# Kernel optimization log

Measured on AMD Instinct MI355X. Metric: run time of the kernel, lower is better.

The kernel has to match this reference:

```python
import jax, jax.numpy as jnp
import numpy as np

B, T, CH, V, E, L = 64, 1024, 256, 32000, 64, 128  # batch, enc_len, channel, vocab, emb_dim, latent_dims


def setup_inputs() -> dict:
    key = jax.random.key(0)
    ks = jax.random.split(key, 13)
    s = 0.05  # weight init scale
    return {
        "prev_cont_vec": jax.random.normal(ks[0], (B, CH), jnp.float32),
        "F": jax.random.normal(ks[1], (B, T, CH), jnp.float32),
        "prev_char": jax.random.normal(ks[2], (B, V), jnp.float32),
        "state_h": jax.random.normal(ks[3], (B, L), jnp.float32),
        "state_c": jax.random.normal(ks[4], (B, L), jnp.float32),
        # learned parameters (all Dense layers use_bias=False)
        "Wc": jax.random.normal(ks[5], (V, E), jnp.float32) * s,
        "Wct1": jax.random.normal(ks[6], (CH, E), jnp.float32) * s,
        "Wo": jax.random.normal(ks[7], (L, V), jnp.float32) * s,
        "Wct2": jax.random.normal(ks[8], (CH, V), jnp.float32) * s,
        "lstm_kernel": jax.random.normal(ks[9], (E, 4 * L), jnp.float32) * s,
        "lstm_recurrent": jax.random.normal(ks[10], (L, 4 * L), jnp.float32) * s,
        "W_h": jax.random.normal(ks[11], (L, CH), jnp.float32) * s,
        "V_attn": jax.random.normal(ks[12], (1, 1, CH), jnp.float32) * s,
    }


def reference(prev_cont_vec, F, prev_char, state_h, state_c,
              Wc, Wct1, Wo, Wct2, lstm_kernel, lstm_recurrent, W_h, V_attn):
    # lstm input: Wc(prev_char) + Wct1(prev_cont_vec)  -> [B, E]
    lstm_inp = prev_char @ Wc + prev_cont_vec @ Wct1
    # Keras LSTMCell (no bias), gate order i, f, c, o
    z = lstm_inp @ lstm_kernel + state_h @ lstm_recurrent  # [B, 4L]
    zi, zf, zg, zo = jnp.split(z, 4, axis=-1)
    i = jax.nn.sigmoid(zi)
    f = jax.nn.sigmoid(zf)
    g = jnp.tanh(zg)
    o = jax.nn.sigmoid(zo)
    new_c = f * state_c + i * g
    new_h = o * jnp.tanh(new_c)
    # training=True branch: clip returned cell state
    new_c_out = jnp.clip(new_c, -10.0, 10.0)
    # additive attention over time axis of F [B, T, CH]
    H_tfm = (new_h @ W_h)[:, None, :]            # [B, 1, CH]
    e_t = V_attn * jnp.tanh(H_tfm + F)           # [B, T, CH]
    attn = jax.nn.softmax(e_t, axis=1)           # softmax over T, per channel
    c_t = jnp.sum(attn * F, axis=1)              # [B, CH]
    # output distribution
    O_t = jax.nn.softmax(new_h @ Wo + c_t @ Wct2, axis=1)  # [B, V]
    return (O_t, c_t, new_h, new_c_out)
```

## Files before the change

kernel.cpp:

```cpp
#include <hip/hip_runtime.h>
#include <hip/hip_bf16.h>

#define BB 64
#define TT 1024
#define CHN 256
#define VV 32000
#define EE 64
#define LL 128
#define NC1 250
#define KC1 128
#define TS 32
#define NV5 500

typedef unsigned short u16;
typedef unsigned int u32;
typedef __attribute__((ext_vector_type(8))) short short8;
typedef __attribute__((ext_vector_type(16))) float f32x16;

__device__ __forceinline__ float fast_rcp(float x) { return __builtin_amdgcn_rcpf(x); }
__device__ __forceinline__ float tanh_fast(float y) {
    float e = __expf(2.0f * y);
    return 1.0f - 2.0f * fast_rcp(1.0f + e);
}
__device__ __forceinline__ float sigmoid_fast(float x) {
    return fast_rcp(1.0f + __expf(-x));
}
__device__ __forceinline__ u16 f2bf(float f) {
    u32 u = __float_as_uint(f);
    return (u16)((u + 0x7fffu + ((u >> 16) & 1u)) >> 16);
}
__device__ __forceinline__ u32 pack_bf2(float lo, float hi) {
    return (u32)f2bf(lo) | ((u32)f2bf(hi) << 16);
}
__device__ __forceinline__ float bf2f(u16 x) {
    return __uint_as_float(((u32)x) << 16);
}
__device__ __forceinline__ size_t apk_idx(int g, int b) {
    return ((size_t)(((g >> 3) * 2 + ((g & 7) >> 2)) * 64 + b)) * 4 + (g & 3);
}

__global__ __launch_bounds__(512) void k1_stage1(const float* __restrict__ A,
                                                 const float* __restrict__ Wc,
                                                 float* __restrict__ part) {
    __shared__ float sW[KC1][EE];
    __shared__ float sAT[KC1][64];
    const int kc = blockIdx.x;
    const int k0 = kc * KC1;
    const int t  = threadIdx.x;

    #pragma unroll
    for (int f = t; f < 2048; f += 512)
        *(float4*)(&sW[0][0] + f * 4) = *(const float4*)(Wc + (size_t)k0 * EE + f * 4);
    {
        const int bl = t & 63;
        const int kq = t >> 6;
        const float* src = A + (size_t)bl * VV + k0 + kq * 16;
        #pragma unroll
        for (int j4 = 0; j4 < 4; ++j4) {
            float4 v = *(const float4*)(src + j4 * 4);
            sAT[kq * 16 + j4 * 4 + 0][bl] = v.x;
            sAT[kq * 16 + j4 * 4 + 1][bl] = v.y;
            sAT[kq * 16 + j4 * 4 + 2][bl] = v.z;
            sAT[kq * 16 + j4 * 4 + 3][bl] = v.w;
        }
    }
    __syncthreads();

    const int e  = t & 63;
    const int b0 = (t >> 6) * 8;
    float acc[8];
    #pragma unroll
    for (int i = 0; i < 8; ++i) acc[i] = 0.0f;

    #pragma unroll 4
    for (int k = 0; k < KC1; ++k) {
        float wt = sW[k][e];
        float4 a0 = *(const float4*)&sAT[k][b0];
        float4 a1 = *(const float4*)&sAT[k][b0 + 4];
        acc[0] = fmaf(a0.x, wt, acc[0]);
        acc[1] = fmaf(a0.y, wt, acc[1]);
        acc[2] = fmaf(a0.z, wt, acc[2]);
        acc[3] = fmaf(a0.w, wt, acc[3]);
        acc[4] = fmaf(a1.x, wt, acc[4]);
        acc[5] = fmaf(a1.y, wt, acc[5]);
        acc[6] = fmaf(a1.z, wt, acc[6]);
        acc[7] = fmaf(a1.w, wt, acc[7]);
    }
    #pragma unroll
    for (int i = 0; i < 8; ++i)
        part[((size_t)(b0 + i) * NC1 + kc) * EE + e] = acc[i];
}

__global__ __launch_bounds__(512) void k2_lstm(const float* __restrict__ part,
    const float* __restrict__ pcv, const float* __restrict__ state_h,
    const float* __restrict__ state_c, const float* __restrict__ Wct1,
    const float* __restrict__ lstm_kernel, const float* __restrict__ lstm_rec,
    const float* __restrict__ W_h,
    float* __restrict__ out_newh, float* __restrict__ out_newc,
    u32* __restrict__ Apk, float* __restrict__ Htfm) {
    __shared__ float red[8][EE];
    __shared__ float inp[EE];
    __shared__ float sh[LL];
    __shared__ float z[4 * LL];
    __shared__ float nh[LL];
    const int b = blockIdx.x;
    const int t = threadIdx.x;
    const int e  = t & 63;
    const int g  = t >> 6;

    {
        float s = 0.0f;
        #pragma unroll 4
        for (int j = g; j < NC1; j += 8)
            s += part[((size_t)b * NC1 + j) * EE + e];
        const int c0 = g * 32;
        #pragma unroll 8
        for (int c = 0; c < 32; ++c)
            s = fmaf(pcv[b * CHN + c0 + c], Wct1[(size_t)(c0 + c) * EE + e], s);
        red[g][e] = s;
    }
    __syncthreads();
    if (t < EE) {
        float s = 0.0f;
        #pragma unroll
        for (int j = 0; j < 8; ++j) s += red[j][t];
        inp[t] = s;
    } else if (t >= 64 && t < 64 + LL) {
        sh[t - 64] = state_h[b * LL + (t - 64)];
    }
    __syncthreads();
    {
        float a = 0.0f;
        #pragma unroll 8
        for (int e2 = 0; e2 < EE; ++e2) a = fmaf(inp[e2], lstm_kernel[e2 * 512 + t], a);
        #pragma unroll 8
        for (int l = 0; l < LL; ++l) a = fmaf(sh[l], lstm_rec[l * 512 + t], a);
        z[t] = a;
    }
    __syncthreads();
    if (t < LL) {
        float zi = z[t], zf = z[LL + t], zg = z[2 * LL + t], zo = z[3 * LL + t];
        float ig = sigmoid_fast(zi);
        float fg = sigmoid_fast(zf);
        float gg = tanh_fast(zg);
        float og = sigmoid_fast(zo);
        float co = state_c[b * LL + t];
        float cn = fg * co + ig * gg;
        float hn = og * tanh_fast(cn);
        out_newc[b * LL + t] = fminf(fmaxf(cn, -10.0f), 10.0f);
        out_newh[b * LL + t] = hn;
        nh[t] = hn;
    }
    __syncthreads();
    if (t < CHN) {
        float a = 0.0f;
        #pragma unroll 8
        for (int l = 0; l < LL; ++l) a = fmaf(nh[l], W_h[l * CHN + t], a);
        Htfm[b * CHN + t] = a;
    } else if (t >= CHN && t < CHN + 64) {
        const int gp = t - CHN;
        Apk[apk_idx(gp, b)] = pack_bf2(nh[2 * gp], nh[2 * gp + 1]);
    }
}

__global__ __launch_bounds__(256) void k3_attn(const float* __restrict__ F,
    const float* __restrict__ Htfm, const float* __restrict__ Vattn,
    float* __restrict__ pS, float* __restrict__ pW) {
    __shared__ float4 sS[256];
    __shared__ float4 sW[256];
    const int b    = blockIdx.x;
    const int ts   = blockIdx.y;
    const int lane = threadIdx.x & 63;
    const int w    = threadIdx.x >> 6;
    const int ch   = lane * 4;

    float4 h = *(const float4*)(Htfm + b * CHN + ch);
    float4 v = *(const float4*)(Vattn + ch);
    float s0 = 0, s1 = 0, s2 = 0, s3 = 0;
    float a0 = 0, a1 = 0, a2 = 0, a3 = 0;

    const float* Fp = F + ((size_t)b * TT + ts * (TT / TS) + w * 8) * CHN + ch;
    float4 cur = *(const float4*)(Fp);
    #pragma unroll
    for (int t = 0; t < 8; ++t) {
        float4 nxt;
        if (t < 7) nxt = *(const float4*)(Fp + (size_t)(t + 1) * CHN);
        float e0 = __expf(v.x * tanh_fast(h.x + cur.x));
        float e1 = __expf(v.y * tanh_fast(h.y + cur.y));
        float e2 = __expf(v.z * tanh_fast(h.z + cur.z));
        float e3 = __expf(v.w * tanh_fast(h.w + cur.w));
        s0 += e0; s1 += e1; s2 += e2; s3 += e3;
        a0 = fmaf(e0, cur.x, a0); a1 = fmaf(e1, cur.y, a1);
        a2 = fmaf(e2, cur.z, a2); a3 = fmaf(e3, cur.w, a3);
        cur = nxt;
    }
    sS[threadIdx.x] = make_float4(s0, s1, s2, s3);
    sW[threadIdx.x] = make_float4(a0, a1, a2, a3);
    __syncthreads();
    if (threadIdx.x < 64) {
        float4 S = sS[threadIdx.x];
        float4 W = sW[threadIdx.x];
        #pragma unroll
        for (int j = 1; j < 4; ++j) {
            float4 s = sS[j * 64 + threadIdx.x];
            float4 q = sW[j * 64 + threadIdx.x];
            S.x += s.x; S.y += s.y; S.z += s.z; S.w += s.w;
            W.x += q.x; W.y += q.y; W.z += q.z; W.w += q.w;
        }
        int base = (b * TS + ts) * CHN + threadIdx.x * 4;
        *(float4*)(pS + base) = S;
        *(float4*)(pW + base) = W;
    }
}

__global__ __launch_bounds__(256) void k4_combine(const float* __restrict__ pS,
    const float* __restrict__ pW, float* __restrict__ out_ct, u32* __restrict__ Apk) {
    __shared__ float sc[CHN];
    const int b = blockIdx.x;
    const int ch = threadIdx.x;
    float S = 0.0f, W = 0.0f;
    #pragma unroll
    for (int j = 0; j < TS; ++j) {
        int idx = (b * TS + j) * CHN + ch;
        S += pS[idx];
        W += pW[idx];
    }
    float c = W / S;
    out_ct[b * CHN + ch] = c;
    sc[ch] = c;
    __syncthreads();
    if (ch < 128)
        Apk[apk_idx(64 + ch, b)] = pack_bf2(sc[2 * ch], sc[2 * ch + 1]);
}

__global__ __launch_bounds__(256) void k5_logits(const float* __restrict__ Wo,
    const float* __restrict__ Wct2, const u32* __restrict__ Apk,
    u16* __restrict__ expb, float* __restrict__ psum) {
    __shared__ float rp[4][32];
    const int t    = threadIdx.x;
    const int lane = t & 63;
    const int wv   = t >> 6;
    const int m    = lane & 31;
    const int kq   = lane >> 5;
    const int vt   = blockIdx.x;
    const int n0   = vt * 64 + (wv >> 1) * 32;
    const int gb0  = (wv & 1) * 32;

    uint4 af[24];
    #pragma unroll
    for (int tt = 0; tt < 24; ++tt)
        af[tt] = *(const uint4*)&Apk[((size_t)((tt * 2 + kq) * 64) + gb0 + m) * 4];

    f32x16 acc = {0.0f, 0.0f, 0.0f, 0.0f, 0.0f, 0.0f, 0.0f, 0.0f,
                  0.0f, 0.0f, 0.0f, 0.0f, 0.0f, 0.0f, 0.0f, 0.0f};

    float wbuf[3][8];
    #pragma unroll
    for (int pf = 0; pf < 2; ++pf) {
        const float* c0 = Wo + (size_t)(pf * 16 + kq * 8) * VV + n0 + m;
        #pragma unroll
        for (int j = 0; j < 8; ++j) wbuf[pf][j] = c0[(size_t)j * VV];
    }

    #pragma unroll
    for (int tt = 0; tt < 24; ++tt) {
        if (tt < 22) {
            const int kn = (tt + 2) * 16 + kq * 8;
            const float* cn = (kn < LL ? Wo + (size_t)kn * VV
                                       : Wct2 + (size_t)(kn - LL) * VV) + n0 + m;
            #pragma unroll
            for (int j = 0; j < 8; ++j) wbuf[(tt + 2) % 3][j] = cn[(size_t)j * VV];
        }
        short8 a, b;
        u32 ax = af[tt].x, ay = af[tt].y, az = af[tt].z, aw = af[tt].w;
        #pragma unroll
        for (int r = 0; r < 4; ++r) {
            u32 lo = __float_as_uint(wbuf[tt % 3][2 * r]);
            u32 hi = __float_as_uint(wbuf[tt % 3][2 * r + 1]);
            u32 bp = (lo >> 16) | (hi & 0xffff0000u);
            u32 ap = (r == 0) ? ax : (r == 1) ? ay : (r == 2) ? az : aw;
            a[2 * r]     = (short)(ap & 0xffff);
            a[2 * r + 1] = (short)(ap >> 16);
            b[2 * r]     = (short)(bp & 0xffff);
            b[2 * r + 1] = (short)(bp >> 16);
        }
        acc = __builtin_amdgcn_mfma_f32_32x32x16_bf16(a, b, acc, 0, 0, 0);
    }

    float ex[16];
    #pragma unroll
    for (int r = 0; r < 16; ++r) {
        const int row = (r & 3) + 8 * (r >> 2) + 4 * kq;
        ex[r] = __expf(acc[r]);
        expb[(size_t)(gb0 + row) * VV + n0 + m] = f2bf(ex[r]);
    }
    #pragma unroll
    for (int r = 0; r < 16; ++r) {
        float s = ex[r];
        s += __shfl_xor(s, 1, 64);  s += __shfl_xor(s, 2, 64);
        s += __shfl_xor(s, 4, 64);  s += __shfl_xor(s, 8, 64);
        s += __shfl_xor(s, 16, 64);
        ex[r] = s;
    }
    if (m == 0) {
        #pragma unroll
        for (int r = 0; r < 16; ++r)
            rp[wv][(r & 3) + 8 * (r >> 2) + 4 * kq] = ex[r];
    }
    __syncthreads();
    if (t < 64) {
        const int hb = t >> 5, r = t & 31;
        psum[(size_t)vt * BB + t] = rp[hb][r] + rp[2 + hb][r];
    }
}

__global__ __launch_bounds__(256) void k5c_norm(const u16* __restrict__ expb,
    const float* __restrict__ psum, float* __restrict__ O) {
    __shared__ float red[256];
    const int b   = blockIdx.x;
    const int seg = blockIdx.y;
    const int t   = threadIdx.x;

    float s = psum[(size_t)t * BB + b];
    if (t + 256 < NV5) s += psum[(size_t)(t + 256) * BB + b];
    red[t] = s;
    __syncthreads();
    #pragma unroll
    for (int off = 128; off > 0; off >>= 1) {
        if (t < off) red[t] += red[t + off];
        __syncthreads();
    }
    const float inv = fast_rcp(red[0]);

    const u16* src = expb + (size_t)b * VV + seg * 4000;
    float* dst     = O + (size_t)b * VV + seg * 4000;
    #pragma unroll 2
    for (int i = t; i < 1000; i += 256) {
        uint2 pk = *(const uint2*)(src + i * 4);
        float4 f;
        f.x = bf2f((u16)(pk.x & 0xffff)) * inv;
        f.y = bf2f((u16)(pk.x >> 16)) * inv;
        f.z = bf2f((u16)(pk.y & 0xffff)) * inv;
        f.w = bf2f((u16)(pk.y >> 16)) * inv;
        *(float4*)(dst + i * 4) = f;
    }
}

extern "C" void kernel_launch(void* const* d_in, const int* in_sizes, int n_in,
                              void* d_out, int out_size, void* d_ws, size_t ws_size,
                              hipStream_t stream) {
    (void)in_sizes; (void)n_in; (void)out_size; (void)ws_size;
    const float* pcv       = (const float*)d_in[0];
    const float* F         = (const float*)d_in[1];
    const float* prev_char = (const float*)d_in[2];
    const float* state_h   = (const float*)d_in[3];
    const float* state_c   = (const float*)d_in[4];
    const float* Wc        = (const float*)d_in[5];
    const float* Wct1      = (const float*)d_in[6];
    const float* Wo        = (const float*)d_in[7];
    const float* Wct2      = (const float*)d_in[8];
    const float* lstm_k    = (const float*)d_in[9];
    const float* lstm_r    = (const float*)d_in[10];
    const float* W_h       = (const float*)d_in[11];
    const float* Vattn     = (const float*)d_in[12];

    float* outO  = (float*)d_out;
    float* outCt = outO + (size_t)BB * VV;
    float* outH  = outCt + (size_t)BB * CHN;
    float* outC  = outH + (size_t)BB * LL;

    float* ws     = (float*)d_ws;
    float* part   = ws;
    float* pS     = part + (size_t)NC1 * BB * EE;
    float* pW     = pS + (size_t)BB * TS * CHN;
    float* Htfm   = pW + (size_t)BB * TS * CHN;
    float* psum   = Htfm + (size_t)BB * CHN;
    u32*   Apk    = (u32*)(psum + (size_t)NV5 * BB);
    u16*   expb   = (u16*)(Apk + 12288);

    hipLaunchKernelGGL(k1_stage1, dim3(NC1), dim3(512), 0, stream, prev_char, Wc, part);
    hipLaunchKernelGGL(k2_lstm, dim3(BB), dim3(512), 0, stream, part, pcv, state_h,
                       state_c, Wct1, lstm_k, lstm_r, W_h, outH, outC, Apk, Htfm);
    hipLaunchKernelGGL(k3_attn, dim3(BB, TS), dim3(256), 0, stream, F, Htfm, Vattn, pS, pW);
    hipLaunchKernelGGL(k4_combine, dim3(BB), dim3(256), 0, stream, pS, pW, outCt, Apk);
    hipLaunchKernelGGL(k5_logits, dim3(NV5), dim3(256), 0, stream, Wo, Wct2, Apk, expb, psum);
    hipLaunchKernelGGL(k5c_norm, dim3(BB, 8), dim3(256), 0, stream, expb, psum, outO);
}
```

Baseline: 226.2 us.

## Fuse all six stages into one cooperative persistent kernel with grid syncs

Replaces the six separate kernel launches with one cooperative kernel of 256 blocks × 512 threads that runs each stage in turn, separated by grid.sync(). The attention stage is re-tiled from 32 time splits to 4, so each thread handles 32 timesteps, and the logits and normalize stages pack two work units per block. The goal is to remove launch overhead and the gaps between kernels. In exchange, several stages use only 64 of the 256 blocks, and each grid-wide barrier has its own cost.

```diff
diff --git a/kernel.cpp b/kernel.cpp
--- a/kernel.cpp
+++ b/kernel.cpp
@@ -1,5 +1,7 @@
 #include <hip/hip_runtime.h>
-#include <hip/hip_bf16.h>
+#include <hip/hip_cooperative_groups.h>
+
+namespace cg = cooperative_groups;
 
 #define BB 64
 #define TT 1024
@@ -9,8 +11,10 @@
 #define LL 128
 #define NC1 250
 #define KC1 128
-#define TS 32
+#define TS4 4
 #define NV5 500
+#define NBLK 256
+#define NTHR 512
 
 typedef unsigned short u16;
 typedef unsigned int u32;
@@ -39,310 +43,322 @@
     return ((size_t)(((g >> 3) * 2 + ((g & 7) >> 2)) * 64 + b)) * 4 + (g & 3);
 }
 
-__global__ __launch_bounds__(512) void k1_stage1(const float* __restrict__ A,
-                                                 const float* __restrict__ Wc,
-                                                 float* __restrict__ part) {
-    __shared__ float sW[KC1][EE];
-    __shared__ float sAT[KC1][64];
-    const int kc = blockIdx.x;
-    const int k0 = kc * KC1;
-    const int t  = threadIdx.x;
-
-    #pragma unroll
-    for (int f = t; f < 2048; f += 512)
-        *(float4*)(&sW[0][0] + f * 4) = *(const float4*)(Wc + (size_t)k0 * EE + f * 4);
-    {
-        const int bl = t & 63;
-        const int kq = t >> 6;
-        const float* src = A + (size_t)bl * VV + k0 + kq * 16;
-        #pragma unroll
-        for (int j4 = 0; j4 < 4; ++j4) {
-            float4 v = *(const float4*)(src + j4 * 4);
-            sAT[kq * 16 + j4 * 4 + 0][bl] = v.x;
-            sAT[kq * 16 + j4 * 4 + 1][bl] = v.y;
-            sAT[kq * 16 + j4 * 4 + 2][bl] = v.z;
-            sAT[kq * 16 + j4 * 4 + 3][bl] = v.w;
-        }
-    }
-    __syncthreads();
-
-    const int e  = t & 63;
-    const int b0 = (t >> 6) * 8;
-    float acc[8];
-    #pragma unroll
-    for (int i = 0; i < 8; ++i) acc[i] = 0.0f;
-
-    #pragma unroll 4
-    for (int k = 0; k < KC1; ++k) {
-        float wt = sW[k][e];
-        float4 a0 = *(const float4*)&sAT[k][b0];
-        float4 a1 = *(const float4*)&sAT[k][b0 + 4];
-        acc[0] = fmaf(a0.x, wt, acc[0]);
-        acc[1] = fmaf(a0.y, wt, acc[1]);
-        acc[2] = fmaf(a0.z, wt, acc[2]);
-        acc[3] = fmaf(a0.w, wt, acc[3]);
-        acc[4] = fmaf(a1.x, wt, acc[4]);
-        acc[5] = fmaf(a1.y, wt, acc[5]);
-        acc[6] = fmaf(a1.z, wt, acc[6]);
-        acc[7] = fmaf(a1.w, wt, acc[7]);
-    }
-    #pragma unroll
-    for (int i = 0; i < 8; ++i)
-        part[((size_t)(b0 + i) * NC1 + kc) * EE + e] = acc[i];
-}
-
-__global__ __launch_bounds__(512) void k2_lstm(const float* __restrict__ part,
+__global__ __launch_bounds__(NTHR, 2) void fused(
+    const float* __restrict__ prev_char, const float* __restrict__ Wc,
     const float* __restrict__ pcv, const float* __restrict__ state_h,
     const float* __restrict__ state_c, const float* __restrict__ Wct1,
     const float* __restrict__ lstm_kernel, const float* __restrict__ lstm_rec,
-    const float* __restrict__ W_h,
-    float* __restrict__ out_newh, float* __restrict__ out_newc,
-    u32* __restrict__ Apk, float* __restrict__ Htfm) {
-    __shared__ float red[8][EE];
-    __shared__ float inp[EE];
-    __shared__ float sh[LL];
-    __shared__ float z[4 * LL];
-    __shared__ float nh[LL];
-    const int b = blockIdx.x;
-    const int t = threadIdx.x;
-    const int e  = t & 63;
-    const int g  = t >> 6;
+    const float* __restrict__ W_h, const float* __restrict__ F,
+    const float* __restrict__ Vattn, const float* __restrict__ Wo,
+    const float* __restrict__ Wct2,
+    float* __restrict__ outO, float* __restrict__ outCt,
+    float* __restrict__ outH, float* __restrict__ outC,
+    float* __restrict__ part, float* __restrict__ pS, float* __restrict__ pW,
+    float* __restrict__ Htfm, float* __restrict__ psum,
+    u32* __restrict__ Apk, u16* __restrict__ expb) {
+
+    __shared__ __align__(16) char smem[65536];
+    cg::grid_group grid = cg::this_grid();
+    const int blk = blockIdx.x;
+    const int t   = threadIdx.x;
+
+    if (blk < NC1) {
+        float (*sW1)[EE] = (float (*)[EE])smem;
+        float (*sAT)[64] = (float (*)[64])(smem + 32768);
+        const int k0 = blk * KC1;
+
+        #pragma unroll
+        for (int f = t; f < 2048; f += NTHR)
+            *(float4*)(&sW1[0][0] + f * 4) = *(const float4*)(Wc + (size_t)k0 * EE + f * 4);
+        {
+            const int bl = t & 63;
+            const int kq = t >> 6;
+            const float* src = prev_char + (size_t)bl * VV + k0 + kq * 16;
+            #pragma unroll
+            for (int j4 = 0; j4 < 4; ++j4) {
+                float4 v = *(const float4*)(src + j4 * 4);
+                sAT[kq * 16 + j4 * 4 + 0][bl] = v.x;
+                sAT[kq * 16 + j4 * 4 + 1][bl] = v.y;
+                sAT[kq * 16 + j4 * 4 + 2][bl] = v.z;
+                sAT[kq * 16 + j4 * 4 + 3][bl] = v.w;
+            }
+        }
+        __syncthreads();
+
+        const int e  = t & 63;
+        const int b0 = (t >> 6) * 8;
+        float acc[8];
+        #pragma unroll
+        for (int i = 0; i < 8; ++i) acc[i] = 0.0f;
+
+        #pragma unroll 4
+        for (int k = 0; k < KC1; ++k) {
+            float wt = sW1[k][e];
+            float4 a0 = *(const float4*)&sAT[k][b0];
+            float4 a1 = *(const float4*)&sAT[k][b0 + 4];
+            acc[0] = fmaf(a0.x, wt, acc[0]);
+            acc[1] = fmaf(a0.y, wt, acc[1]);
+            acc[2] = fmaf(a0.z, wt, acc[2]);
+            acc[3] = fmaf(a0.w, wt, acc[3]);
+            acc[4] = fmaf(a1.x, wt, acc[4]);
+            acc[5] = fmaf(a1.y, wt, acc[5]);
+            acc[6] = fmaf(a1.z, wt, acc[6]);
+            acc[7] = fmaf(a1.w, wt, acc[7]);
+        }
+        #pragma unroll
+        for (int i = 0; i < 8; ++i)
+            part[((size_t)(b0 + i) * NC1 + blk) * EE + e] = acc[i];
+    }
+    grid.sync();
+
+    if (blk < BB) {
+        float (*red)[EE] = (float (*)[EE])smem;
+        float* inp = (float*)(smem + 8 * EE * 4);
+        float* sh  = inp + EE;
+        float* z   = sh + LL;
+        float* nh  = z + 4 * LL;
+        const int b = blk;
+        const int e = t & 63;
+        const int g = t >> 6;
+
+        {
+            float s = 0.0f;
+            #pragma unroll 4
+            for (int j = g; j < NC1; j += 8)
+                s += part[((size_t)b * NC1 + j) * EE + e];
+            const int c0 = g * 32;
+            #pragma unroll 8
+            for (int c = 0; c < 32; ++c)
+                s = fmaf(pcv[b * CHN + c0 + c], Wct1[(size_t)(c0 + c) * EE + e], s);
+            red[g][e] = s;
+        }
+        __syncthreads();
+        if (t < EE) {
+            float s = 0.0f;
+            #pragma unroll
+            for (int j = 0; j < 8; ++j) s += red[j][t];
+            inp[t] = s;
+        } else if (t >= 64 && t < 64 + LL) {
+            sh[t - 64] = state_h[b * LL + (t - 64)];
+        }
+        __syncthreads();
+        {
+            float a = 0.0f;
+            #pragma unroll 8
+            for (int e2 = 0; e2 < EE; ++e2) a = fmaf(inp[e2], lstm_kernel[e2 * 512 + t], a);
+            #pragma unroll 8
+            for (int l = 0; l < LL; ++l) a = fmaf(sh[l], lstm_rec[l * 512 + t], a);
+            z[t] = a;
+        }
+        __syncthreads();
+        if (t < LL) {
+            float zi = z[t], zf = z[LL + t], zg = z[2 * LL + t], zo = z[3 * LL + t];
+            float ig = sigmoid_fast(zi);
+            float fg = sigmoid_fast(zf);
+            float gg = tanh_fast(zg);
+            float og = sigmoid_fast(zo);
+            float co = state_c[b * LL + t];
+            float cn = fg * co + ig * gg;
+            float hn = og * tanh_fast(cn);
+            outC[b * LL + t] = fminf(fmaxf(cn, -10.0f), 10.0f);
+            outH[b * LL + t] = hn;
+            nh[t] = hn;
+        }
+        __syncthreads();
+        if (t < CHN) {
+            float a = 0.0f;
+            #pragma unroll 8
+            for (int l = 0; l < LL; ++l) a = fmaf(nh[l], W_h[l * CHN + t], a);
+            Htfm[b * CHN + t] = a;
+        } else if (t >= CHN && t < CHN + 64) {
+            const int gp = t - CHN;
+            Apk[apk_idx(gp, b)] = pack_bf2(nh[2 * gp], nh[2 * gp + 1]);
+        }
+    }
+    grid.sync();
 
     {
-        float s = 0.0f;
-        #pragma unroll 4
-        for (int j = g; j < NC1; j += 8)
-            s += part[((size_t)b * NC1 + j) * EE + e];
-        const int c0 = g * 32;
-        #pragma unroll 8
-        for (int c = 0; c < 32; ++c)
-            s = fmaf(pcv[b * CHN + c0 + c], Wct1[(size_t)(c0 + c) * EE + e], s);
-        red[g][e] = s;
-    }
-    __syncthreads();
-    if (t < EE) {
-        float s = 0.0f;
-        #pragma unroll
-        for (int j = 0; j < 8; ++j) s += red[j][t];
-        inp[t] = s;
-    } else if (t >= 64 && t < 64 + LL) {
-        sh[t - 64] = state_h[b * LL + (t - 64)];
-    }
-    __syncthreads();
+        float4* sS4 = (float4*)smem;
+        float4* sW4 = sS4 + NTHR;
+        const int b    = blk >> 2;
+        const int ts   = blk & 3;
+        const int lane = t & 63;
+        const int w    = t >> 6;
+        const int ch   = lane * 4;
+
+        float4 h4 = *(const float4*)(Htfm + b * CHN + ch);
+        float4 v4 = *(const float4*)(Vattn + ch);
+        float s0 = 0, s1 = 0, s2 = 0, s3 = 0;
+        float a0 = 0, a1 = 0, a2 = 0, a3 = 0;
+
+        const float* Fp = F + ((size_t)b * TT + ts * 256 + w * 32) * CHN + ch;
+        float4 cur = *(const float4*)(Fp);
+        #pragma unroll
+        for (int q = 0; q < 32; ++q) {
+            float4 nxt;
+            if (q < 31) nxt = *(const float4*)(Fp + (size_t)(q + 1) * CHN);
+            float e0 = __expf(v4.x * tanh_fast(h4.x + cur.x));
+            float e1 = __expf(v4.y * tanh_fast(h4.y + cur.y));
+            float e2 = __expf(v4.z * tanh_fast(h4.z + cur.z));
+            float e3 = __expf(v4.w * tanh_fast(h4.w + cur.w));
+            s0 += e0; s1 += e1; s2 += e2; s3 += e3;
+            a0 = fmaf(e0, cur.x, a0); a1 = fmaf(e1, cur.y, a1);
+            a2 = fmaf(e2, cur.z, a2); a3 = fmaf(e3, cur.w, a3);
+            cur = nxt;
+        }
+        sS4[t] = make_float4(s0, s1, s2, s3);
+        sW4[t] = make_float4(a0, a1, a2, a3);
+        __syncthreads();
+        if (t < 64) {
+            float4 S = sS4[t];
+            float4 W4 = sW4[t];
+            #pragma unroll
+            for (int j = 1; j < 8; ++j) {
+                float4 s = sS4[j * 64 + t];
+                float4 q = sW4[j * 64 + t];
+                S.x += s.x; S.y += s.y; S.z += s.z; S.w += s.w;
+                W4.x += q.x; W4.y += q.y; W4.z += q.z; W4.w += q.w;
+            }
+            int base = (b * TS4 + ts) * CHN + t * 4;
+            *(float4*)(pS + base) = S;
+            *(float4*)(pW + base) = W4;
+        }
+    }
+    grid.sync();
+
+    if (blk < BB) {
+        float* sc = (float*)smem;
+        const int b = blk;
+        if (t < CHN) {
+            float S = 0.0f, W = 0.0f;
+            #pragma unroll
+            for (int j = 0; j < TS4; ++j) {
+                int idx = (b * TS4 + j) * CHN + t;
+                S += pS[idx];
+                W += pW[idx];
+            }
+            float c = W / S;
+            outCt[b * CHN + t] = c;
+            sc[t] = c;
+        }
+        __syncthreads();
+        if (t < 128)
+            Apk[apk_idx(64 + t, b)] = pack_bf2(sc[2 * t], sc[2 * t + 1]);
+    }
+    grid.sync();
+
+    if (blk < NC1) {
+        float (*rp)[4][32] = (float (*)[4][32])smem;
+        const int sub  = t >> 8;
+        const int tid  = t & 255;
+        const int lane = tid & 63;
+        const int wv   = tid >> 6;
+        const int m    = lane & 31;
+        const int kq   = lane >> 5;
+        const int vt   = blk * 2 + sub;
+        const int n0   = vt * 64 + (wv >> 1) * 32;
+        const int gb0  = (wv & 1) * 32;
+
+        uint4 af[24];
+        #pragma unroll
+        for (int tt = 0; tt < 24; ++tt)
+            af[tt] = *(const uint4*)&Apk[((size_t)((tt * 2 + kq) * 64) + gb0 + m) * 4];
+
+        f32x16 acc = {0.0f, 0.0f, 0.0f, 0.0f, 0.0f, 0.0f, 0.0f, 0.0f,
+                      0.0f, 0.0f, 0.0f, 0.0f, 0.0f, 0.0f, 0.0f, 0.0f};
+
+        float wbuf[3][8];
+        #pragma unroll
+        for (int pf = 0; pf < 2; ++pf) {
+            const float* c0 = Wo + (size_t)(pf * 16 + kq * 8) * VV + n0 + m;
+            #pragma unroll
+            for (int j = 0; j < 8; ++j) wbuf[pf][j] = c0[(size_t)j * VV];
+        }
+
+        #pragma unroll
+        for (int tt = 0; tt < 24; ++tt) {
+            if (tt < 22) {
+                const int kn = (tt + 2) * 16 + kq * 8;
+                const float* cn = (kn < LL ? Wo + (size_t)kn * VV
+                                           : Wct2 + (size_t)(kn - LL) * VV) + n0 + m;
+                #pragma unroll
+                for (int j = 0; j < 8; ++j) wbuf[(tt + 2) % 3][j] = cn[(size_t)j * VV];
+            }
+            short8 a, b;
+            u32 ax = af[tt].x, ay = af[tt].y, az = af[tt].z, aw = af[tt].w;
+            #pragma unroll
+            for (int r = 0; r < 4; ++r) {
+                u32 lo = __float_as_uint(wbuf[tt % 3][2 * r]);
+                u32 hi = __float_as_uint(wbuf[tt % 3][2 * r + 1]);
+                u32 bp = (lo >> 16) | (hi & 0xffff0000u);
+                u32 ap = (r == 0) ? ax : (r == 1) ? ay : (r == 2) ? az : aw;
+                a[2 * r]     = (short)(ap & 0xffff);
+                a[2 * r + 1] = (short)(ap >> 16);
+                b[2 * r]     = (short)(bp & 0xffff);
+                b[2 * r + 1] = (short)(bp >> 16);
+            }
+            acc = __builtin_amdgcn_mfma_f32_32x32x16_bf16(a, b, acc, 0, 0, 0);
+        }
+
+        float ex[16];
+        #pragma unroll
+        for (int r = 0; r < 16; ++r) {
+            const int row = (r & 3) + 8 * (r >> 2) + 4 * kq;
+            ex[r] = __expf(acc[r]);
+            expb[(size_t)(gb0 + row) * VV + n0 + m] = f2bf(ex[r]);
+        }
+        #pragma unroll
+        for (int r = 0; r < 16; ++r) {
+            float s = ex[r];
+            s += __shfl_xor(s, 1, 64);  s += __shfl_xor(s, 2, 64);
+            s += __shfl_xor(s, 4, 64);  s += __shfl_xor(s, 8, 64);
+            s += __shfl_xor(s, 16, 64);
+            ex[r] = s;
+        }
+        if (m == 0) {
+            #pragma unroll
+            for (int r = 0; r < 16; ++r)
+                rp[sub][wv][(r & 3) + 8 * (r >> 2) + 4 * kq] = ex[r];
+        }
+        __syncthreads();
+        if (tid < 64) {
+            const int hb = tid >> 5, r = tid & 31;
+            psum[(size_t)vt * BB + tid] = rp[sub][hb][r] + rp[sub][2 + hb][r];
+        }
+    }
+    grid.sync();
+
     {
-        float a = 0.0f;
-        #pragma unroll 8
-        for (int e2 = 0; e2 < EE; ++e2) a = fmaf(inp[e2], lstm_kernel[e2 * 512 + t], a);
-        #pragma unroll 8
-        for (int l = 0; l < LL; ++l) a = fmaf(sh[l], lstm_rec[l * 512 + t], a);
-        z[t] = a;
-    }
-    __syncthreads();
-    if (t < LL) {
-        float zi = z[t], zf = z[LL + t], zg = z[2 * LL + t], zo = z[3 * LL + t];
-        float ig = sigmoid_fast(zi);
-        float fg = sigmoid_fast(zf);
-        float gg = tanh_fast(zg);
-        float og = sigmoid_fast(zo);
-        float co = state_c[b * LL + t];
-        float cn = fg * co + ig * gg;
-        float hn = og * tanh_fast(cn);
-        out_newc[b * LL + t] = fminf(fmaxf(cn, -10.0f), 10.0f);
-        out_newh[b * LL + t] = hn;
-        nh[t] = hn;
-    }
-    __syncthreads();
-    if (t < CHN) {
-        float a = 0.0f;
-        #pragma unroll 8
-        for (int l = 0; l < LL; ++l) a = fmaf(nh[l], W_h[l * CHN + t], a);
-        Htfm[b * CHN + t] = a;
-    } else if (t >= CHN && t < CHN + 64) {
-        const int gp = t - CHN;
-        Apk[apk_idx(gp, b)] = pack_bf2(nh[2 * gp], nh[2 * gp + 1]);
-    }
-}
-
-__global__ __launch_bounds__(256) void k3_attn(const float* __restrict__ F,
-    const float* __restrict__ Htfm, const float* __restrict__ Vattn,
-    float* __restrict__ pS, float* __restrict__ pW) {
-    __shared__ float4 sS[256];
-    __shared__ float4 sW[256];
-    const int b    = blockIdx.x;
-    const int ts   = blockIdx.y;
-    const int lane = threadIdx.x & 63;
-    const int w    = threadIdx.x >> 6;
-    const int ch   = lane * 4;
-
-    float4 h = *(const float4*)(Htfm + b * CHN + ch);
-    float4 v = *(const float4*)(Vattn + ch);
-    float s0 = 0, s1 = 0, s2 = 0, s3 = 0;
-    float a0 = 0, a1 = 0, a2 = 0, a3 = 0;
-
-    const float* Fp = F + ((size_t)b * TT + ts * (TT / TS) + w * 8) * CHN + ch;
-    float4 cur = *(const float4*)(Fp);
-    #pragma unroll
-    for (int t = 0; t < 8; ++t) {
-        float4 nxt;
-        if (t < 7) nxt = *(const float4*)(Fp + (size_t)(t + 1) * CHN);
-        float e0 = __expf(v.x * tanh_fast(h.x + cur.x));
-        float e1 = __expf(v.y * tanh_fast(h.y + cur.y));
-        float e2 = __expf(v.z * tanh_fast(h.z + cur.z));
-        float e3 = __expf(v.w * tanh_fast(h.w + cur.w));
-        s0 += e0; s1 += e1; s2 += e2; s3 += e3;
-        a0 = fmaf(e0, cur.x, a0); a1 = fmaf(e1, cur.y, a1);
-        a2 = fmaf(e2, cur.z, a2); a3 = fmaf(e3, cur.w, a3);
-        cur = nxt;
-    }
-    sS[threadIdx.x] = make_float4(s0, s1, s2, s3);
-    sW[threadIdx.x] = make_float4(a0, a1, a2, a3);
-    __syncthreads();
-    if (threadIdx.x < 64) {
-        float4 S = sS[threadIdx.x];
-        float4 W = sW[threadIdx.x];
-        #pragma unroll
-        for (int j = 1; j < 4; ++j) {
-            float4 s = sS[j * 64 + threadIdx.x];
-            float4 q = sW[j * 64 + threadIdx.x];
-            S.x += s.x; S.y += s.y; S.z += s.z; S.w += s.w;
-            W.x += q.x; W.y += q.y; W.z += q.z; W.w += q.w;
-        }
-        int base = (b * TS + ts) * CHN + threadIdx.x * 4;
-        *(float4*)(pS + base) = S;
-        *(float4*)(pW + base) = W;
-    }
-}
-
-__global__ __launch_bounds__(256) void k4_combine(const float* __restrict__ pS,
-    const float* __restrict__ pW, float* __restrict__ out_ct, u32* __restrict__ Apk) {
-    __shared__ float sc[CHN];
-    const int b = blockIdx.x;
-    const int ch = threadIdx.x;
-    float S = 0.0f, W = 0.0f;
-    #pragma unroll
-    for (int j = 0; j < TS; ++j) {
-        int idx = (b * TS + j) * CHN + ch;
-        S += pS[idx];
-        W += pW[idx];
-    }
-    float c = W / S;
-    out_ct[b * CHN + ch] = c;
-    sc[ch] = c;
-    __syncthreads();
-    if (ch < 128)
-        Apk[apk_idx(64 + ch, b)] = pack_bf2(sc[2 * ch], sc[2 * ch + 1]);
-}
-
-__global__ __launch_bounds__(256) void k5_logits(const float* __restrict__ Wo,
-    const float* __restrict__ Wct2, const u32* __restrict__ Apk,
-    u16* __restrict__ expb, float* __restrict__ psum) {
-    __shared__ float rp[4][32];
-    const int t    = threadIdx.x;
-    const int lane = t & 63;
-    const int wv   = t >> 6;
-    const int m    = lane & 31;
-    const int kq   = lane >> 5;
-    const int vt   = blockIdx.x;
-    const int n0   = vt * 64 + (wv >> 1) * 32;
-    const int gb0  = (wv & 1) * 32;
-
-    uint4 af[24];
-    #pragma unroll
-    for (int tt = 0; tt < 24; ++tt)
-        af[tt] = *(const uint4*)&Apk[((size_t)((tt * 2 + kq) * 64) + gb0 + m) * 4];
-
-    f32x16 acc = {0.0f, 0.0f, 0.0f, 0.0f, 0.0f, 0.0f, 0.0f, 0.0f,
-                  0.0f, 0.0f, 0.0f, 0.0f, 0.0f, 0.0f, 0.0f, 0.0f};
-
-    float wbuf[3][8];
-    #pragma unroll
-    for (int pf = 0; pf < 2; ++pf) {
-        const float* c0 = Wo + (size_t)(pf * 16 + kq * 8) * VV + n0 + m;
-        #pragma unroll
-        for (int j = 0; j < 8; ++j) wbuf[pf][j] = c0[(size_t)j * VV];
-    }
-
-    #pragma unroll
-    for (int tt = 0; tt < 24; ++tt) {
-        if (tt < 22) {
-            const int kn = (tt + 2) * 16 + kq * 8;
-            const float* cn = (kn < LL ? Wo + (size_t)kn * VV
-                                       : Wct2 + (size_t)(kn - LL) * VV) + n0 + m;
-            #pragma unroll
-            for (int j = 0; j < 8; ++j) wbuf[(tt + 2) % 3][j] = cn[(size_t)j * VV];
-        }
-        short8 a, b;
-        u32 ax = af[tt].x, ay = af[tt].y, az = af[tt].z, aw = af[tt].w;
-        #pragma unroll
-        for (int r = 0; r < 4; ++r) {
-            u32 lo = __float_as_uint(wbuf[tt % 3][2 * r]);
-            u32 hi = __float_as_uint(wbuf[tt % 3][2 * r + 1]);
-            u32 bp = (lo >> 16) | (hi & 0xffff0000u);
-            u32 ap = (r == 0) ? ax : (r == 1) ? ay : (r == 2) ? az : aw;
-            a[2 * r]     = (short)(ap & 0xffff);
-            a[2 * r + 1] = (short)(ap >> 16);
-            b[2 * r]     = (short)(bp & 0xffff);
-            b[2 * r + 1] = (short)(bp >> 16);
-        }
-        acc = __builtin_amdgcn_mfma_f32_32x32x16_bf16(a, b, acc, 0, 0, 0);
-    }
-
-    float ex[16];
-    #pragma unroll
-    for (int r = 0; r < 16; ++r) {
-        const int row = (r & 3) + 8 * (r >> 2) + 4 * kq;
-        ex[r] = __expf(acc[r]);
-        expb[(size_t)(gb0 + row) * VV + n0 + m] = f2bf(ex[r]);
-    }
-    #pragma unroll
-    for (int r = 0; r < 16; ++r) {
-        float s = ex[r];
-        s += __shfl_xor(s, 1, 64);  s += __shfl_xor(s, 2, 64);
-        s += __shfl_xor(s, 4, 64);  s += __shfl_xor(s, 8, 64);
-        s += __shfl_xor(s, 16, 64);
-        ex[r] = s;
-    }
-    if (m == 0) {
-        #pragma unroll
-        for (int r = 0; r < 16; ++r)
-            rp[wv][(r & 3) + 8 * (r >> 2) + 4 * kq] = ex[r];
-    }
-    __syncthreads();
-    if (t < 64) {
-        const int hb = t >> 5, r = t & 31;
-        psum[(size_t)vt * BB + t] = rp[hb][r] + rp[2 + hb][r];
-    }
-}
-
-__global__ __launch_bounds__(256) void k5c_norm(const u16* __restrict__ expb,
-    const float* __restrict__ psum, float* __restrict__ O) {
-    __shared__ float red[256];
-    const int b   = blockIdx.x;
-    const int seg = blockIdx.y;
-    const int t   = threadIdx.x;
-
-    float s = psum[(size_t)t * BB + b];
-    if (t + 256 < NV5) s += psum[(size_t)(t + 256) * BB + b];
-    red[t] = s;
-    __syncthreads();
-    #pragma unroll
-    for (int off = 128; off > 0; off >>= 1) {
-        if (t < off) red[t] += red[t + off];
-        __syncthreads();
-    }
-    const float inv = fast_rcp(red[0]);
-
-    const u16* src = expb + (size_t)b * VV + seg * 4000;
-    float* dst     = O + (size_t)b * VV + seg * 4000;
-    #pragma unroll 2
-    for (int i = t; i < 1000; i += 256) {
-        uint2 pk = *(const uint2*)(src + i * 4);
-        float4 f;
-        f.x = bf2f((u16)(pk.x & 0xffff)) * inv;
-        f.y = bf2f((u16)(pk.x >> 16)) * inv;
-        f.z = bf2f((u16)(pk.y & 0xffff)) * inv;
-        f.w = bf2f((u16)(pk.y >> 16)) * inv;
-        *(float4*)(dst + i * 4) = f;
+        float (*red6)[256] = (float (*)[256])smem;
+        const int sub  = t >> 8;
+        const int tid  = t & 255;
+        const int unit = blk * 2 + sub;
+        const int b    = unit >> 3;
+        const int seg  = unit & 7;
+
+        float s = psum[(size_t)tid * BB + b];
+        if (tid + 256 < NV5) s += psum[(size_t)(tid + 256) * BB + b];
+        red6[sub][tid] = s;
+        __syncthreads();
+        #pragma unroll
+        for (int off = 128; off > 0; off >>= 1) {
+            if (tid < off) red6[sub][tid] += red6[sub][tid + off];
+            __syncthreads();
+        }
+        const float inv = fast_rcp(red6[sub][0]);
+
+        const u16* src = expb + (size_t)b * VV + seg * 4000;
+        float* dst     = outO + (size_t)b * VV + seg * 4000;
+        #pragma unroll 2
+        for (int i = tid; i < 1000; i += 256) {
+            uint2 pk = *(const uint2*)(src + i * 4);
+            float4 f;
+            f.x = bf2f((u16)(pk.x & 0xffff)) * inv;
+            f.y = bf2f((u16)(pk.x >> 16)) * inv;
+            f.z = bf2f((u16)(pk.y & 0xffff)) * inv;
+            f.w = bf2f((u16)(pk.y >> 16)) * inv;
+            *(float4*)(dst + i * 4) = f;
+        }
     }
 }
 
@@ -372,17 +388,20 @@
     float* ws     = (float*)d_ws;
     float* part   = ws;
     float* pS     = part + (size_t)NC1 * BB * EE;
-    float* pW     = pS + (size_t)BB * TS * CHN;
-    float* Htfm   = pW + (size_t)BB * TS * CHN;
+    float* pW     = pS + (size_t)BB * TS4 * CHN;
+    float* Htfm   = pW + (size_t)BB * TS4 * CHN;
     float* psum   = Htfm + (size_t)BB * CHN;
     u32*   Apk    = (u32*)(psum + (size_t)NV5 * BB);
     u16*   expb   = (u16*)(Apk + 12288);
 
-    hipLaunchKernelGGL(k1_stage1, dim3(NC1), dim3(512), 0, stream, prev_char, Wc, part);
-    hipLaunchKernelGGL(k2_lstm, dim3(BB), dim3(512), 0, stream, part, pcv, state_h,
-                       state_c, Wct1, lstm_k, lstm_r, W_h, outH, outC, Apk, Htfm);
-    hipLaunchKernelGGL(k3_attn, dim3(BB, TS), dim3(256), 0, stream, F, Htfm, Vattn, pS, pW);
-    hipLaunchKernelGGL(k4_combine, dim3(BB), dim3(256), 0, stream, pS, pW, outCt, Apk);
-    hipLaunchKernelGGL(k5_logits, dim3(NV5), dim3(256), 0, stream, Wo, Wct2, Apk, expb, psum);
-    hipLaunchKernelGGL(k5c_norm, dim3(BB, 8), dim3(256), 0, stream, expb, psum, outO);
-}
+    void* args[] = {
+        (void*)&prev_char, (void*)&Wc, (void*)&pcv, (void*)&state_h, (void*)&state_c,
+        (void*)&Wct1, (void*)&lstm_k, (void*)&lstm_r, (void*)&W_h, (void*)&F,
+        (void*)&Vattn, (void*)&Wo, (void*)&Wct2,
+        (void*)&outO, (void*)&outCt, (void*)&outH, (void*)&outC,
+        (void*)&part, (void*)&pS, (void*)&pW, (void*)&Htfm, (void*)&psum,
+        (void*)&Apk, (void*)&expb
+    };
+    hipLaunchCooperativeKernel((const void*)fused, dim3(NBLK), dim3(NTHR),
+                               args, 0, stream);
+}
```

Measured after the change: 378.4 us. 1.67x slower.
